# Kernel tuning notes

Hardware: AMD Instinct MI355X
Metric: run time of the kernel (lower is better)

The kernel has to match this reference:

```python
import jax, jax.numpy as jnp
import numpy as np

B, S, HID = 1, 2048, 2880
NH, NKV, D = 64, 8, 64
G = NH // NKV          # GQA group size = 8
SW = 128               # sliding window
SCALE = D ** -0.5
NEG = -1e30


def rotate_half(x):
    h = x.shape[-1] // 2
    return jnp.concatenate([-x[..., h:], x[..., :h]], axis=-1)


def setup_inputs() -> dict:
    key = jax.random.key(0)
    ks = jax.random.split(key, 11)
    hidden_states = jax.random.normal(ks[0], (B, S, HID), dtype=jnp.float32)
    # RoPE tables [S, D]
    inv_freq = 1.0 / (10000.0 ** (np.arange(0, D, 2, dtype=np.float32) / D))
    freqs = np.arange(S, dtype=np.float32)[:, None] * inv_freq[None, :]
    emb = np.concatenate([freqs, freqs], axis=-1)
    cos = jnp.asarray(np.cos(emb), dtype=jnp.float32)
    sin = jnp.asarray(np.sin(emb), dtype=jnp.float32)
    std = 0.02
    wq = jax.random.normal(ks[1], (HID, NH * D), dtype=jnp.float32) * std
    bq = jax.random.normal(ks[2], (NH * D,), dtype=jnp.float32) * std
    wk = jax.random.normal(ks[3], (HID, NKV * D), dtype=jnp.float32) * std
    bk = jax.random.normal(ks[4], (NKV * D,), dtype=jnp.float32) * std
    wv = jax.random.normal(ks[5], (HID, NKV * D), dtype=jnp.float32) * std
    bv = jax.random.normal(ks[6], (NKV * D,), dtype=jnp.float32) * std
    wo = jax.random.normal(ks[7], (NH * D, HID), dtype=jnp.float32) * std
    bo = jax.random.normal(ks[8], (HID,), dtype=jnp.float32) * std
    sinks = jax.random.normal(ks[9], (NH,), dtype=jnp.float32)
    return dict(hidden_states=hidden_states, cos=cos, sin=sin, wq=wq, bq=bq,
                wk=wk, bk=bk, wv=wv, bv=bv, wo=wo, bo=bo, sinks=sinks)


def reference(hidden_states, cos, sin, wq, bq, wk, bk, wv, bv, wo, bo, sinks):
    b, s, _ = hidden_states.shape
    q = (hidden_states @ wq + bq).reshape(b, s, NH, D)
    k = (hidden_states @ wk + bk).reshape(b, s, NKV, D)
    v = (hidden_states @ wv + bv).reshape(b, s, NKV, D)
    # RoPE (rotate-half), cos/sin broadcast over batch and heads
    c = cos[None, :, None, :]
    si = sin[None, :, None, :]
    q = q * c + rotate_half(q) * si
    k = k * c + rotate_half(k) * si
    # GQA: [b, s, kv, g, d]
    qg = q.reshape(b, s, NKV, G, D)
    # scores [b, kv, g, q, s]
    scores = jnp.einsum('bqkgd,bskd->bkgqs', qg, k) * SCALE
    i = jnp.arange(s)
    allowed = (i[:, None] >= i[None, :]) & (i[:, None] - i[None, :] < SW)
    scores = jnp.where(allowed[None, None, None], scores, NEG)
    # sink softmax: per-head learnable logit added to the denominator only
    sink = sinks.reshape(NKV, G)[None, :, :, None]            # [1, kv, g, 1]
    m = jnp.maximum(scores.max(axis=-1), sink)                # [b, kv, g, q]
    e = jnp.exp(scores - m[..., None])
    denom = e.sum(axis=-1) + jnp.exp(sink - m)                # sink absorbs mass
    p = e / denom[..., None]
    attn = jnp.einsum('bkgqs,bskd->bqkgd', p, v).reshape(b, s, NH * D)
    return attn @ wo + bo
```

## Files before the change

### kernel.cpp

```cpp
#include <hip/hip_runtime.h>
#include <hip/hip_bf16.h>
#include <stdint.h>

#define S_LEN 2048
#define HID 2880
#define NH 64
#define NKV 8
#define HD 64
#define NQ (NH * HD)
#define NKVD (NKV * HD)
#define SCALE 0.125f

typedef unsigned short u16;
typedef __attribute__((ext_vector_type(8))) short short8;
typedef __attribute__((ext_vector_type(4))) float floatx4;

__device__ __forceinline__ u16 f2bf(float f) {
  union { float f; unsigned u; } x; x.f = f;
  unsigned r = x.u + 0x7fffu + ((x.u >> 16) & 1u);
  return (u16)(r >> 16);
}

__device__ __forceinline__ int xcd_swz(int orig, int nwg) {
  int q = nwg >> 3, r = nwg & 7, xcd = orig & 7, lid = orig >> 3;
  return (xcd < r ? xcd * (q + 1) : r * (q + 1) + (xcd - r) * q) + lid;
}

__device__ __forceinline__ void gl2lds16(const void* g, void* l) {
  __builtin_amdgcn_global_load_lds(
      (__attribute__((address_space(1))) unsigned int*)(uintptr_t)g,
      (__attribute__((address_space(3))) unsigned int*)(unsigned int)(uintptr_t)l,
      16, 0, 0);
}

__global__ void k_convert(const float* __restrict__ in, u16* __restrict__ out, int n4) {
  int i = blockIdx.x * blockDim.x + threadIdx.x;
  if (i >= n4) return;
  float4 v = *((const float4*)in + i);
  ushort4 o;
  o.x = f2bf(v.x); o.y = f2bf(v.y); o.z = f2bf(v.z); o.w = f2bf(v.w);
  *(ushort4*)(out + (size_t)i * 4) = o;
}

__global__ void k_transpose_all(const float* __restrict__ wq, const float* __restrict__ wk,
                                const float* __restrict__ wv, const float* __restrict__ wo,
                                u16* __restrict__ wqt, u16* __restrict__ wkt,
                                u16* __restrict__ wvt, u16* __restrict__ wot) {
  __shared__ float tile[32][33];
  int b = blockIdx.x;
  const int nwq = (NQ / 32) * (HID / 32);
  const int nwkv = (NKVD / 32) * (HID / 32);
  const float* in; u16* out; int R, C, bx, by;
  if (b < nwq) {
    in = wq; out = wqt; R = HID; C = NQ;
    int nx = NQ / 32; bx = (b % nx) * 32; by = (b / nx) * 32;
  } else if (b < nwq + nwkv) {
    b -= nwq; in = wk; out = wkt; R = HID; C = NKVD;
    int nx = NKVD / 32; bx = (b % nx) * 32; by = (b / nx) * 32;
  } else if (b < nwq + 2 * nwkv) {
    b -= nwq + nwkv; in = wv; out = wvt; R = HID; C = NKVD;
    int nx = NKVD / 32; bx = (b % nx) * 32; by = (b / nx) * 32;
  } else {
    b -= nwq + 2 * nwkv; in = wo; out = wot; R = NQ; C = HID;
    int nx = HID / 32; bx = (b % nx) * 32; by = (b / nx) * 32;
  }
  int tx = threadIdx.x, ty = threadIdx.y;
#pragma unroll
  for (int i = 0; i < 4; ++i)
    tile[ty + i * 8][tx] = in[(long)(by + ty + i * 8) * C + bx + tx];
  __syncthreads();
#pragma unroll
  for (int i = 0; i < 4; ++i)
    out[(long)(bx + ty + i * 8) * R + by + tx] = f2bf(tile[tx][ty + i * 8]);
}

__device__ __forceinline__ void gemm_tile(const u16* __restrict__ Abase, int lda,
                                          const u16* __restrict__ Bbase, int ldb,
                                          int kloop, floatx4 acc[4][4]) {
  __shared__ __align__(16) u16 As[3][128][32];
  __shared__ __align__(16) u16 Bs[3][128][32];
  const int t = threadIdx.x;
  const int w = t >> 6, l = t & 63;
  const int srow = w * 16 + (l >> 2);
  const int scol = (((l & 3) ^ ((l >> 3) & 3))) * 8;
  const int wr = (w >> 1) * 64, wc = (w & 1) * 64;
  const int fr = l & 15;
  const int fk8 = (((l >> 4) ^ ((l >> 1) & 3))) * 8;
  floatx4 zero = {0.f, 0.f, 0.f, 0.f};
#pragma unroll
  for (int i = 0; i < 4; ++i)
#pragma unroll
    for (int j = 0; j < 4; ++j) acc[i][j] = zero;

  const u16* Ar0 = Abase + (long)srow * lda + scol;
  const u16* Ar1 = Abase + (long)(64 + srow) * lda + scol;
  const u16* Br0 = Bbase + (long)srow * ldb + scol;
  const u16* Br1 = Bbase + (long)(64 + srow) * ldb + scol;

#define STAGE(buf, kt) do {                              \
    long ko_ = (long)(kt) * 32;                          \
    gl2lds16(Ar0 + ko_, &As[buf][w * 16][0]);            \
    gl2lds16(Ar1 + ko_, &As[buf][64 + w * 16][0]);       \
    gl2lds16(Br0 + ko_, &Bs[buf][w * 16][0]);            \
    gl2lds16(Br1 + ko_, &Bs[buf][64 + w * 16][0]);       \
  } while (0)

  const int nk = kloop >> 5;
  STAGE(0, 0);
  STAGE(1, 1);
  int cur = 0, nxt = 1, fut = 2;
  for (int kt = 0; kt < nk; ++kt) {
    if (kt + 1 < nk) { asm volatile("s_waitcnt vmcnt(4)" ::: "memory"); }
    else             { asm volatile("s_waitcnt vmcnt(0)" ::: "memory"); }
    asm volatile("s_barrier" ::: "memory");
    if (kt + 2 < nk) STAGE(fut, kt + 2);
    short8 af[4], bf8[4];
#pragma unroll
    for (int i = 0; i < 4; ++i) af[i] = *(const short8*)&As[cur][wr + i * 16 + fr][fk8];
#pragma unroll
    for (int j = 0; j < 4; ++j) bf8[j] = *(const short8*)&Bs[cur][wc + j * 16 + fr][fk8];
#pragma unroll
    for (int i = 0; i < 4; ++i)
#pragma unroll
      for (int j = 0; j < 4; ++j)
        acc[i][j] = __builtin_amdgcn_mfma_f32_16x16x32_bf16(af[i], bf8[j], acc[i][j], 0, 0, 0);
    int tmp = cur; cur = nxt; nxt = fut; fut = tmp;
  }
#undef STAGE
}

__device__ __forceinline__ void gemm_tile8(const u16* __restrict__ Abase, int lda,
                                           const u16* __restrict__ Bbase, int ldb,
                                           int kloop, floatx4 acc[2][4]) {
  __shared__ __align__(16) u16 As[3][128][32];
  __shared__ __align__(16) u16 Bs[3][128][32];
  const int t = threadIdx.x;
  const int w = t >> 6, l = t & 63;
  const int srow = w * 16 + (l >> 2);
  const int scol = (((l & 3) ^ ((l >> 3) & 3))) * 8;
  const int wr = (w >> 1) * 32, wc = (w & 1) * 64;
  const int fr = l & 15;
  const int fk8 = (((l >> 4) ^ ((l >> 1) & 3))) * 8;
  floatx4 zero = {0.f, 0.f, 0.f, 0.f};
#pragma unroll
  for (int i = 0; i < 2; ++i)
#pragma unroll
    for (int j = 0; j < 4; ++j) acc[i][j] = zero;

  const u16* Ar = Abase + (long)srow * lda + scol;
  const u16* Br = Bbase + (long)srow * ldb + scol;

#define STAGE8(buf, kt) do {                             \
    long ko_ = (long)(kt) * 32;                          \
    gl2lds16(Ar + ko_, &As[buf][w * 16][0]);             \
    gl2lds16(Br + ko_, &Bs[buf][w * 16][0]);             \
  } while (0)

  const int nk = kloop >> 5;
  STAGE8(0, 0);
  STAGE8(1, 1);
  int cur = 0, nxt = 1, fut = 2;
  for (int kt = 0; kt < nk; ++kt) {
    if (kt + 1 < nk) { asm volatile("s_waitcnt vmcnt(2)" ::: "memory"); }
    else             { asm volatile("s_waitcnt vmcnt(0)" ::: "memory"); }
    asm volatile("s_barrier" ::: "memory");
    if (kt + 2 < nk) STAGE8(fut, kt + 2);
    short8 af[2], bf8[4];
#pragma unroll
    for (int i = 0; i < 2; ++i) af[i] = *(const short8*)&As[cur][wr + i * 16 + fr][fk8];
#pragma unroll
    for (int j = 0; j < 4; ++j) bf8[j] = *(const short8*)&Bs[cur][wc + j * 16 + fr][fk8];
#pragma unroll
    for (int i = 0; i < 2; ++i)
#pragma unroll
      for (int j = 0; j < 4; ++j)
        acc[i][j] = __builtin_amdgcn_mfma_f32_16x16x32_bf16(af[i], bf8[j], acc[i][j], 0, 0, 0);
    int tmp = cur; cur = nxt; nxt = fut; fut = tmp;
  }
#undef STAGE8
}

__global__ __launch_bounds__(512) void k_gemm_qkv(
    const u16* __restrict__ hsb, const u16* __restrict__ wqt,
    const u16* __restrict__ wkt, const u16* __restrict__ wvt,
    const float* __restrict__ bq, const float* __restrict__ bk, const float* __restrict__ bv,
    const float* __restrict__ cosb, const float* __restrict__ sinb,
    u16* __restrict__ qbuf, u16* __restrict__ kbuf, u16* __restrict__ vtbuf) {
  int xcd = blockIdx.x & 7, lid = blockIdx.x >> 3;
  int bm = ((xcd & 1) * 8 + (lid & 7)) * 128;
  int bn = ((xcd >> 1) * 10 + (lid >> 3)) * 128;
  const u16* Bt; const float* bias;
  if (bn < NQ)              { Bt = wqt + (long)bn * HID;               bias = bq + bn; }
  else if (bn < NQ + NKVD)  { Bt = wkt + (long)(bn - NQ) * HID;        bias = bk + (bn - NQ); }
  else                      { Bt = wvt + (long)(bn - NQ - NKVD) * HID; bias = bv + (bn - NQ - NKVD); }
  floatx4 acc[2][4];
  gemm_tile8(hsb + (long)bm * HID, HID, Bt, HID, HID, acc);
  int t = threadIdx.x, w = t >> 6, l = t & 63;
  int wr = (w >> 1) * 32, wc = (w & 1) * 64, fr = l & 15, fq = (l >> 4) * 4;
  if (bn < NQ + NKVD) {
    int ng0 = bn + wc;
    u16* hbase;
    if (ng0 < NQ) hbase = qbuf + (long)(ng0 >> 6) * S_LEN * HD;
    else          hbase = kbuf + (long)((ng0 - NQ) >> 6) * S_LEN * HD;
#pragma unroll
    for (int i = 0; i < 2; ++i)
#pragma unroll
      for (int r = 0; r < 4; ++r) {
        int srow = bm + wr + i * 16 + fq + r;
        const float* crow = cosb + (long)srow * HD;
        const float* srw  = sinb + (long)srow * HD;
#pragma unroll
        for (int j = 0; j < 2; ++j) {
          int dlo = j * 16 + fr;
          float c  = crow[dlo];
          float si = srw[dlo];
          float xl = acc[i][j][r]     + bias[wc + j * 16 + fr];
          float xh = acc[i][j + 2][r] + bias[wc + (j + 2) * 16 + fr];
          hbase[(long)srow * HD + dlo]      = f2bf(xl * c - xh * si);
          hbase[(long)srow * HD + dlo + 32] = f2bf(xh * c + xl * si);
        }
      }
  } else {
#pragma unroll
    for (int i = 0; i < 2; ++i)
#pragma unroll
      for (int j = 0; j < 4; ++j) {
        int ncol = wc + j * 16 + fr;
        int n3 = bn + ncol - NQ - NKVD;
        float bsv = bias[ncol];
#pragma unroll
        for (int r = 0; r < 4; ++r) {
          int srow = bm + wr + i * 16 + fq + r;
          vtbuf[(long)(n3 >> 6) * HD * S_LEN + (long)(n3 & 63) * S_LEN + srow] =
              f2bf(acc[i][j][r] + bsv);
        }
      }
  }
}

__global__ __launch_bounds__(256) void k_attn(
    const u16* __restrict__ qb, const u16* __restrict__ kb, const u16* __restrict__ vtb,
    const float* __restrict__ sinks, u16* __restrict__ ao) {
  __shared__ __align__(16) u16 Kl[192][72];
  __shared__ __align__(16) u16 Vl[64][200];
  int t = threadIdx.x;
  int h = blockIdx.y, kvh = h >> 3;
  int qs = blockIdx.x * 64;
  int kstart = qs - 128;
  const u16* kbase = kb + (long)kvh * S_LEN * HD;
  const u16* vbase = vtb + (long)kvh * HD * S_LEN;
#pragma unroll
  for (int it = 0; it < 6; ++it) {
    int idx = t + it * 256;
    int c = idx >> 3, dc = (idx & 7) * 8;
    int j = kstart + c;
    short8 v = {0, 0, 0, 0, 0, 0, 0, 0};
    if (j >= 0) v = *(const short8*)(kbase + (long)j * HD + dc);
    *(short8*)&Kl[c][dc] = v;
  }
#pragma unroll
  for (int it = 0; it < 6; ++it) {
    int idx = t + it * 256;
    int d = idx / 24, c8 = idx % 24;
    int c = c8 * 8;
    int j = kstart + c;
    short8 v = {0, 0, 0, 0, 0, 0, 0, 0};
    if (j >= 0) v = *(const short8*)(vbase + (long)d * S_LEN + j);
    *(short8*)&Vl[d][c] = v;
  }
  __syncthreads();

  int w = t >> 6, l = t & 63;
  int fr = l & 15, fk8 = (l >> 4) * 8, fq = (l >> 4) * 4;
  const u16* qrow = qb + (long)h * S_LEN * HD + (long)(qs + w * 16 + fr) * HD;
  short8 a0 = *(const short8*)(qrow + fk8);
  short8 a1 = *(const short8*)(qrow + 32 + fk8);
  floatx4 sc[12];
#pragma unroll
  for (int ct = 0; ct < 12; ++ct) {
    floatx4 z = {0.f, 0.f, 0.f, 0.f};
    short8 b0 = *(const short8*)&Kl[ct * 16 + fr][fk8];
    short8 b1 = *(const short8*)&Kl[ct * 16 + fr][32 + fk8];
    z = __builtin_amdgcn_mfma_f32_16x16x32_bf16(a0, b0, z, 0, 0, 0);
    z = __builtin_amdgcn_mfma_f32_16x16x32_bf16(a1, b1, z, 0, 0, 0);
    sc[ct] = z;
  }
  __syncthreads();

  u16* Pw = &Kl[0][0] + w * 16 * 200;
  float snk = sinks[h];
#pragma unroll
  for (int r = 0; r < 4; ++r) {
    int rloc = w * 16 + fq + r;
    int cmin = rloc + 1;
    int jmin = 128 - qs;
    if (jmin > cmin) cmin = jmin;
    int cmax = rloc + 128;
    float vals[12];
    float mx = snk;
#pragma unroll
    for (int ct = 0; ct < 12; ++ct) {
      int c = ct * 16 + fr;
      float v = (c >= cmin && c <= cmax) ? sc[ct][r] * SCALE : -1e30f;
      vals[ct] = v;
      mx = fmaxf(mx, v);
    }
#pragma unroll
    for (int m = 1; m < 16; m <<= 1) mx = fmaxf(mx, __shfl_xor(mx, m));
    float e[12], sum = 0.f;
#pragma unroll
    for (int ct = 0; ct < 12; ++ct) { e[ct] = __expf(vals[ct] - mx); sum += e[ct]; }
#pragma unroll
    for (int m = 1; m < 16; m <<= 1) sum += __shfl_xor(sum, m);
    sum += __expf(snk - mx);
    float inv = 1.f / sum;
#pragma unroll
    for (int ct = 0; ct < 12; ++ct)
      Pw[(fq + r) * 200 + ct * 16 + fr] = f2bf(e[ct] * inv);
  }
  __syncthreads();

  floatx4 o[4];
  floatx4 zero = {0.f, 0.f, 0.f, 0.f};
#pragma unroll
  for (int cd = 0; cd < 4; ++cd) o[cd] = zero;
#pragma unroll
  for (int kk = 0; kk < 6; ++kk) {
    short8 pa = *(const short8*)(Pw + fr * 200 + kk * 32 + fk8);
#pragma unroll
    for (int cd = 0; cd < 4; ++cd) {
      short8 bv8 = *(const short8*)&Vl[cd * 16 + fr][kk * 32 + fk8];
      o[cd] = __builtin_amdgcn_mfma_f32_16x16x32_bf16(pa, bv8, o[cd], 0, 0, 0);
    }
  }
#pragma unroll
  for (int cd = 0; cd < 4; ++cd)
#pragma unroll
    for (int r = 0; r < 4; ++r) {
      int srow = qs + w * 16 + fq + r;
      ao[(long)srow * NQ + h * HD + cd * 16 + fr] = f2bf(o[cd][r]);
    }
}

__global__ __launch_bounds__(256) void k_gemm_out(
    const u16* __restrict__ attn, const u16* __restrict__ wot,
    const float* __restrict__ bo, float* __restrict__ out) {
  int sw = xcd_swz(blockIdx.x, gridDim.x);
  int bm = (sw & 15) * 128, bn = (sw >> 4) * 128;
  floatx4 acc[4][4];
  gemm_tile(attn + (long)bm * NQ, NQ, wot + (long)bn * NQ, NQ, NQ, acc);
  int t = threadIdx.x, w = t >> 6, l = t & 63;
  int wr = (w >> 1) * 64, wc = (w & 1) * 64, fr = l & 15, fq = (l >> 4) * 4;
#pragma unroll
  for (int i = 0; i < 4; ++i)
#pragma unroll
    for (int j = 0; j < 4; ++j) {
      int ng = bn + wc + j * 16 + fr;
      if (ng >= HID) continue;
      float bsv = bo[ng];
#pragma unroll
      for (int r = 0; r < 4; ++r) {
        int srow = bm + wr + i * 16 + fq + r;
        out[(long)srow * HID + ng] = acc[i][j][r] + bsv;
      }
    }
}

extern "C" void kernel_launch(void* const* d_in, const int* in_sizes, int n_in,
                              void* d_out, int out_size, void* d_ws, size_t ws_size,
                              hipStream_t stream) {
  const float* hs    = (const float*)d_in[0];
  const float* cosb  = (const float*)d_in[1];
  const float* sinb  = (const float*)d_in[2];
  const float* wq    = (const float*)d_in[3];
  const float* bq    = (const float*)d_in[4];
  const float* wk    = (const float*)d_in[5];
  const float* bk    = (const float*)d_in[6];
  const float* wv    = (const float*)d_in[7];
  const float* bv    = (const float*)d_in[8];
  const float* wo    = (const float*)d_in[9];
  const float* bo    = (const float*)d_in[10];
  const float* sinks = (const float*)d_in[11];
  float* out = (float*)d_out;

  char* p = (char*)d_ws;
  u16* hsb   = (u16*)p; p += (size_t)S_LEN * HID * 2;
  u16* wqt   = (u16*)p; p += (size_t)NQ * HID * 2;
  u16* wkt   = (u16*)p; p += (size_t)NKVD * HID * 2;
  u16* wvt   = (u16*)p; p += (size_t)NKVD * HID * 2;
  u16* wot   = (u16*)p; p += (size_t)2944 * NQ * 2;
  u16* qbuf  = (u16*)p; p += (size_t)NH * S_LEN * HD * 2;
  u16* kbuf  = (u16*)p; p += (size_t)NKV * S_LEN * HD * 2;
  u16* vtbuf = (u16*)p; p += (size_t)NKV * HD * S_LEN * 2;
  u16* abuf  = (u16*)p; p += (size_t)S_LEN * NQ * 2;

  const int ntr = (NQ / 32) * (HID / 32) * 2 + (NKVD / 32) * (HID / 32) * 2;
  k_convert<<<(S_LEN * HID / 4 + 255) / 256, 256, 0, stream>>>(hs, hsb, S_LEN * HID / 4);
  k_transpose_all<<<ntr, dim3(32, 8), 0, stream>>>(wq, wk, wv, wo, wqt, wkt, wvt, wot);
  k_gemm_qkv<<<(NQ + 2 * NKVD) / 128 * (S_LEN / 128), 512, 0, stream>>>(
      hsb, wqt, wkt, wvt, bq, bk, bv, cosb, sinb, qbuf, kbuf, vtbuf);
  k_attn<<<dim3(S_LEN / 64, NH), 256, 0, stream>>>(qbuf, kbuf, vtbuf, sinks, abuf);
  k_gemm_out<<<23 * 16, 256, 0, stream>>>(abuf, wot, bo, out);
}
```

Measured before the change: 217.0 us.

## Merge preprocessing kernels and deepen output GEMM K-tile to 64

Fuses the hidden-state bf16 conversion and the weight transposes into one launch, removing a kernel launch and its tail. Rewrites the output projection GEMM to use a 64-wide K tile with double buffering and an XOR swizzle, doing twice the MFMA work per barrier. The pipeline drops from three stages to two and waits on vmcnt(0) every iteration, which may expose more load latency.

New measurement: 202.9 us. -6.5%, faster.

```diff
diff --git a/kernel.cpp b/kernel.cpp
--- a/kernel.cpp
+++ b/kernel.cpp
@@ -33,21 +33,23 @@
       16, 0, 0);
 }
 
-__global__ void k_convert(const float* __restrict__ in, u16* __restrict__ out, int n4) {
-  int i = blockIdx.x * blockDim.x + threadIdx.x;
-  if (i >= n4) return;
-  float4 v = *((const float4*)in + i);
-  ushort4 o;
-  o.x = f2bf(v.x); o.y = f2bf(v.y); o.z = f2bf(v.z); o.w = f2bf(v.w);
-  *(ushort4*)(out + (size_t)i * 4) = o;
-}
-
-__global__ void k_transpose_all(const float* __restrict__ wq, const float* __restrict__ wk,
-                                const float* __restrict__ wv, const float* __restrict__ wo,
-                                u16* __restrict__ wqt, u16* __restrict__ wkt,
-                                u16* __restrict__ wvt, u16* __restrict__ wot) {
+__global__ void k_pre(const float* __restrict__ hs, u16* __restrict__ hsb,
+                      const float* __restrict__ wq, const float* __restrict__ wk,
+                      const float* __restrict__ wv, const float* __restrict__ wo,
+                      u16* __restrict__ wqt, u16* __restrict__ wkt,
+                      u16* __restrict__ wvt, u16* __restrict__ wot) {
+  int b = blockIdx.x;
+  const int ncv = (S_LEN * HID / 4) / 256;
+  if (b < ncv) {
+    int i = b * 256 + threadIdx.x;
+    float4 v = ((const float4*)hs)[i];
+    ushort4 o;
+    o.x = f2bf(v.x); o.y = f2bf(v.y); o.z = f2bf(v.z); o.w = f2bf(v.w);
+    *(ushort4*)(hsb + (size_t)i * 4) = o;
+    return;
+  }
+  b -= ncv;
   __shared__ float tile[32][33];
-  int b = blockIdx.x;
   const int nwq = (NQ / 32) * (HID / 32);
   const int nwkv = (NKVD / 32) * (HID / 32);
   const float* in; u16* out; int R, C, bx, by;
@@ -64,7 +66,7 @@
     b -= nwq + 2 * nwkv; in = wo; out = wot; R = NQ; C = HID;
     int nx = HID / 32; bx = (b % nx) * 32; by = (b / nx) * 32;
   }
-  int tx = threadIdx.x, ty = threadIdx.y;
+  int tx = threadIdx.x & 31, ty = threadIdx.x >> 5;
 #pragma unroll
   for (int i = 0; i < 4; ++i)
     tile[ty + i * 8][tx] = in[(long)(by + ty + i * 8) * C + bx + tx];
@@ -72,61 +74,6 @@
 #pragma unroll
   for (int i = 0; i < 4; ++i)
     out[(long)(bx + ty + i * 8) * R + by + tx] = f2bf(tile[tx][ty + i * 8]);
-}
-
-__device__ __forceinline__ void gemm_tile(const u16* __restrict__ Abase, int lda,
-                                          const u16* __restrict__ Bbase, int ldb,
-                                          int kloop, floatx4 acc[4][4]) {
-  __shared__ __align__(16) u16 As[3][128][32];
-  __shared__ __align__(16) u16 Bs[3][128][32];
-  const int t = threadIdx.x;
-  const int w = t >> 6, l = t & 63;
-  const int srow = w * 16 + (l >> 2);
-  const int scol = (((l & 3) ^ ((l >> 3) & 3))) * 8;
-  const int wr = (w >> 1) * 64, wc = (w & 1) * 64;
-  const int fr = l & 15;
-  const int fk8 = (((l >> 4) ^ ((l >> 1) & 3))) * 8;
-  floatx4 zero = {0.f, 0.f, 0.f, 0.f};
-#pragma unroll
-  for (int i = 0; i < 4; ++i)
-#pragma unroll
-    for (int j = 0; j < 4; ++j) acc[i][j] = zero;
-
-  const u16* Ar0 = Abase + (long)srow * lda + scol;
-  const u16* Ar1 = Abase + (long)(64 + srow) * lda + scol;
-  const u16* Br0 = Bbase + (long)srow * ldb + scol;
-  const u16* Br1 = Bbase + (long)(64 + srow) * ldb + scol;
-
-#define STAGE(buf, kt) do {                              \
-    long ko_ = (long)(kt) * 32;                          \
-    gl2lds16(Ar0 + ko_, &As[buf][w * 16][0]);            \
-    gl2lds16(Ar1 + ko_, &As[buf][64 + w * 16][0]);       \
-    gl2lds16(Br0 + ko_, &Bs[buf][w * 16][0]);            \
-    gl2lds16(Br1 + ko_, &Bs[buf][64 + w * 16][0]);       \
-  } while (0)
-
-  const int nk = kloop >> 5;
-  STAGE(0, 0);
-  STAGE(1, 1);
-  int cur = 0, nxt = 1, fut = 2;
-  for (int kt = 0; kt < nk; ++kt) {
-    if (kt + 1 < nk) { asm volatile("s_waitcnt vmcnt(4)" ::: "memory"); }
-    else             { asm volatile("s_waitcnt vmcnt(0)" ::: "memory"); }
-    asm volatile("s_barrier" ::: "memory");
-    if (kt + 2 < nk) STAGE(fut, kt + 2);
-    short8 af[4], bf8[4];
-#pragma unroll
-    for (int i = 0; i < 4; ++i) af[i] = *(const short8*)&As[cur][wr + i * 16 + fr][fk8];
-#pragma unroll
-    for (int j = 0; j < 4; ++j) bf8[j] = *(const short8*)&Bs[cur][wc + j * 16 + fr][fk8];
-#pragma unroll
-    for (int i = 0; i < 4; ++i)
-#pragma unroll
-      for (int j = 0; j < 4; ++j)
-        acc[i][j] = __builtin_amdgcn_mfma_f32_16x16x32_bf16(af[i], bf8[j], acc[i][j], 0, 0, 0);
-    int tmp = cur; cur = nxt; nxt = fut; fut = tmp;
-  }
-#undef STAGE
 }
 
 __device__ __forceinline__ void gemm_tile8(const u16* __restrict__ Abase, int lda,
@@ -345,12 +292,67 @@
 __global__ __launch_bounds__(256) void k_gemm_out(
     const u16* __restrict__ attn, const u16* __restrict__ wot,
     const float* __restrict__ bo, float* __restrict__ out) {
+  __shared__ __align__(16) u16 As[2][128][64];
+  __shared__ __align__(16) u16 Bs[2][128][64];
+  const int t = threadIdx.x;
+  const int w = t >> 6, l = t & 63;
+  const int sr = l >> 3;
+  const int ss = ((l & 7) ^ sr) * 8;
+  const int wr = (w >> 1) * 64, wc = (w & 1) * 64;
+  const int fr = l & 15, g = l >> 4, fq = g * 4;
+  const int fsw = fr & 7;
+
   int sw = xcd_swz(blockIdx.x, gridDim.x);
   int bm = (sw & 15) * 128, bn = (sw >> 4) * 128;
+  const u16* Ar = attn + (long)bm * NQ;
+  const u16* Br = wot + (long)bn * NQ;
+
   floatx4 acc[4][4];
-  gemm_tile(attn + (long)bm * NQ, NQ, wot + (long)bn * NQ, NQ, NQ, acc);
-  int t = threadIdx.x, w = t >> 6, l = t & 63;
-  int wr = (w >> 1) * 64, wc = (w & 1) * 64, fr = l & 15, fq = (l >> 4) * 4;
+  floatx4 zero = {0.f, 0.f, 0.f, 0.f};
+#pragma unroll
+  for (int i = 0; i < 4; ++i)
+#pragma unroll
+    for (int j = 0; j < 4; ++j) acc[i][j] = zero;
+
+#define OSTAGE(buf, kt) do {                                          \
+    long ko_ = (long)(kt) * 64 + ss;                                  \
+    _Pragma("unroll")                                                 \
+    for (int c8 = 0; c8 < 4; ++c8) {                                  \
+      int r0 = w * 32 + c8 * 8;                                       \
+      gl2lds16(Ar + (long)(r0 + sr) * NQ + ko_, &As[buf][r0][0]);     \
+      gl2lds16(Br + (long)(r0 + sr) * NQ + ko_, &Bs[buf][r0][0]);     \
+    } } while (0)
+
+  const int nk = NQ >> 6;
+  OSTAGE(0, 0);
+  for (int kt = 0; kt < nk; ++kt) {
+    const int cb = kt & 1;
+    asm volatile("s_waitcnt vmcnt(0)" ::: "memory");
+    asm volatile("s_barrier" ::: "memory");
+    if (kt + 1 < nk) OSTAGE(cb ^ 1, kt + 1);
+    short8 af[4][2], bf8[4][2];
+#pragma unroll
+    for (int i = 0; i < 4; ++i)
+#pragma unroll
+      for (int kk = 0; kk < 2; ++kk)
+        af[i][kk] = *(const short8*)&As[cb][wr + i * 16 + fr][((kk * 4 + g) ^ fsw) * 8];
+#pragma unroll
+    for (int j = 0; j < 4; ++j)
+#pragma unroll
+      for (int kk = 0; kk < 2; ++kk)
+        bf8[j][kk] = *(const short8*)&Bs[cb][wc + j * 16 + fr][((kk * 4 + g) ^ fsw) * 8];
+#pragma unroll
+    for (int i = 0; i < 4; ++i)
+#pragma unroll
+      for (int j = 0; j < 4; ++j)
+#pragma unroll
+        for (int kk = 0; kk < 2; ++kk)
+          acc[i][j] = __builtin_amdgcn_mfma_f32_16x16x32_bf16(
+              af[i][kk], bf8[j][kk], acc[i][j], 0, 0, 0);
+  }
+#undef OSTAGE
+
+  int fqe = (l >> 4) * 4;
 #pragma unroll
   for (int i = 0; i < 4; ++i)
 #pragma unroll
@@ -360,7 +362,7 @@
       float bsv = bo[ng];
 #pragma unroll
       for (int r = 0; r < 4; ++r) {
-        int srow = bm + wr + i * 16 + fq + r;
+        int srow = bm + wr + i * 16 + fqe + r;
         out[(long)srow * HID + ng] = acc[i][j][r] + bsv;
       }
     }
@@ -394,9 +396,9 @@
   u16* vtbuf = (u16*)p; p += (size_t)NKV * HD * S_LEN * 2;
   u16* abuf  = (u16*)p; p += (size_t)S_LEN * NQ * 2;
 
-  const int ntr = (NQ / 32) * (HID / 32) * 2 + (NKVD / 32) * (HID / 32) * 2;
-  k_convert<<<(S_LEN * HID / 4 + 255) / 256, 256, 0, stream>>>(hs, hsb, S_LEN * HID / 4);
-  k_transpose_all<<<ntr, dim3(32, 8), 0, stream>>>(wq, wk, wv, wo, wqt, wkt, wvt, wot);
+  const int npre = (S_LEN * HID / 4) / 256 +
+                   (NQ / 32) * (HID / 32) * 2 + (NKVD / 32) * (HID / 32) * 2;
+  k_pre<<<npre, 256, 0, stream>>>(hs, hsb, wq, wk, wv, wo, wqt, wkt, wvt, wot);
   k_gemm_qkv<<<(NQ + 2 * NKVD) / 128 * (S_LEN / 128), 512, 0, stream>>>(
       hsb, wqt, wkt, wvt, bq, bk, bv, cosb, sinb, qbuf, kbuf, vtbuf);
   k_attn<<<dim3(S_LEN / 64, NH), 256, 0, stream>>>(qbuf, kbuf, vtbuf, sinks, abuf);
```
